# Kernel tuning notes

Measured on AMD Instinct MI355X. Metric: run time of the kernel, lower is better.

Reference implementation:

```python
import jax, jax.numpy as jnp
import numpy as np

B, H, W, C = 32, 56, 56, 192
NUM_HEADS = 6
WS = 7
SHIFT = 3
HIDDEN = 4 * C


def _relative_position_index(ws):
    coords = np.stack(np.meshgrid(np.arange(ws), np.arange(ws), indexing="ij"))  # 2,ws,ws
    coords = coords.reshape(2, -1)
    rel = coords[:, :, None] - coords[:, None, :]  # 2,N,N
    rel = rel.transpose(1, 2, 0)
    rel[:, :, 0] += ws - 1
    rel[:, :, 1] += ws - 1
    rel[:, :, 0] *= 2 * ws - 1
    return rel.sum(-1)  # N,N in [0, (2ws-1)^2)


def setup_inputs() -> dict:
    key = jax.random.key(0)
    ks = jax.random.split(key, 16)
    s = 0.02
    inp = {
        "x": jax.random.normal(ks[0], (B, H, W, C), jnp.float32),
        "norm1_g": jnp.ones((C,), jnp.float32),
        "norm1_b": jnp.zeros((C,), jnp.float32),
        "qkv_w": jax.random.normal(ks[1], (3 * C, C), jnp.float32) * s,
        "qkv_b": jnp.zeros((3 * C,), jnp.float32),
        "proj_w": jax.random.normal(ks[2], (C, C), jnp.float32) * s,
        "proj_b": jnp.zeros((C,), jnp.float32),
        "rel_bias_table": jax.random.normal(ks[3], ((2 * WS - 1) ** 2, NUM_HEADS), jnp.float32) * s,
        "norm2_g": jnp.ones((C,), jnp.float32),
        "norm2_b": jnp.zeros((C,), jnp.float32),
        "fc1_w": jax.random.normal(ks[4], (HIDDEN, C), jnp.float32) * s,
        "fc1_b": jnp.zeros((HIDDEN,), jnp.float32),
        "fc2_w": jax.random.normal(ks[5], (C, HIDDEN), jnp.float32) * s,
        "fc2_b": jnp.zeros((C,), jnp.float32),
        "rel_index": jnp.asarray(_relative_position_index(WS), jnp.int32),  # (49,49)
    }
    return inp


def _layernorm(x, g, b, eps=1e-5):
    mu = x.mean(-1, keepdims=True)
    var = ((x - mu) ** 2).mean(-1, keepdims=True)
    return (x - mu) * jax.lax.rsqrt(var + eps) * g + b


def _window_partition(x, ws):
    b, h, w, c = x.shape
    x = x.reshape(b, h // ws, ws, w // ws, ws, c)
    return x.transpose(0, 1, 3, 2, 4, 5).reshape(-1, ws * ws, c)


def _window_reverse(win, ws, b, h, w):
    c = win.shape[-1]
    x = win.reshape(b, h // ws, w // ws, ws, ws, c)
    return x.transpose(0, 1, 3, 2, 4, 5).reshape(b, h, w, c)


def reference(x, norm1_g, norm1_b, qkv_w, qkv_b, proj_w, proj_b, rel_bias_table,
              norm2_g, norm2_b, fc1_w, fc1_b, fc2_w, fc2_b, rel_index):
    shortcut = x
    xn = _layernorm(x, norm1_g, norm1_b)
    xs = jnp.roll(xn, (-SHIFT, -SHIFT), axis=(1, 2))
    win = _window_partition(xs, WS)  # (nW*B, 49, C)
    nw, n, c = win.shape
    hd = c // NUM_HEADS
    qkv = win @ qkv_w.T + qkv_b  # (nw, n, 3C)
    qkv = qkv.reshape(nw, n, 3, NUM_HEADS, hd).transpose(2, 0, 3, 1, 4)
    q, k, v = qkv[0], qkv[1], qkv[2]  # (nw, heads, n, hd)
    q = q * (hd ** -0.5)
    attn = jnp.einsum("whnd,whmd->whnm", q, k)
    bias = rel_bias_table[rel_index.reshape(-1)].reshape(n, n, NUM_HEADS).transpose(2, 0, 1)
    attn = jax.nn.softmax(attn + bias[None], axis=-1)
    out = jnp.einsum("whnm,whmd->whnd", attn, v)
    out = out.transpose(0, 2, 1, 3).reshape(nw, n, c)
    out = out @ proj_w.T + proj_b
    xs = _window_reverse(out, WS, x.shape[0], x.shape[1], x.shape[2])
    xa = jnp.roll(xs, (SHIFT, SHIFT), axis=(1, 2))
    x = shortcut + xa
    xm = _layernorm(x, norm2_g, norm2_b)
    xm = jax.nn.gelu(xm @ fc1_w.T + fc1_b, approximate=False)
    xm = xm @ fc2_w.T + fc2_b
    return x + xm
```

## Files before the change

kernel.cpp:

```cpp
#include <hip/hip_runtime.h>
#include <hip/hip_bf16.h>

#define CC 192
#define NHEADS 6
#define HDIM 32
#define NTOK 49
#define NWIN 2048
#define MTOK 100352
#define HIDDEN 768

typedef __hip_bfloat16 bf16;
typedef __attribute__((ext_vector_type(8))) short short8;
typedef __attribute__((ext_vector_type(4))) float f32x4;

__global__ __launch_bounds__(256) void k_wconv(
    const float* __restrict__ qw, const float* __restrict__ pw,
    const float* __restrict__ f1, const float* __restrict__ f2,
    bf16* __restrict__ o) {
  int i = blockIdx.x * 256 + threadIdx.x;
  if (i < 110592) o[i] = __float2bfloat16(qw[i]);
  else if (i < 147456) o[i] = __float2bfloat16(pw[i - 110592]);
  else if (i < 294912) o[i] = __float2bfloat16(f1[i - 147456]);
  else if (i < 442368) o[i] = __float2bfloat16(f2[i - 294912]);
}

__global__ __launch_bounds__(256) void k_bias(
    const float* __restrict__ table, const int* __restrict__ ridx,
    float* __restrict__ bias6) {
  int i = blockIdx.x * 256 + threadIdx.x;
  if (i >= 6 * 2401) return;
  int h = i / 2401, e = i - h * 2401;
  bias6[i] = table[ridx[e] * NHEADS + h];
}

template <int MODE, int NT, int KC, int MF>
__global__ __launch_bounds__(256) void k_gemm_areg(
    const void* __restrict__ Ap, const bf16* __restrict__ W,
    const float* __restrict__ bias, void* __restrict__ out0,
    const void* __restrict__ aux, const float* __restrict__ lng,
    const float* __restrict__ lnb) {
  constexpr int K = KC * 192;
  constexpr int N = NT * 64;
  __shared__ bf16 Bs[2][64 * 192];
  const int tid = threadIdx.x;
  const int wave = tid >> 6, lane = tid & 63;
  const int grp = lane >> 4, rA = lane & 15;
  const int cq = grp, cn = rA;
  const int m0 = blockIdx.x * (MF * 64);
  const int mrow = m0 + wave * (MF * 16);

  short8 areg[MF][KC * 6];
  if constexpr (MODE == 1) {
#pragma unroll
    for (int mt = 0; mt < MF; ++mt) {
      const bf16* arow =
          (const bf16*)Ap + (size_t)(mrow + mt * 16 + rA) * K + grp * 8;
#pragma unroll
      for (int kt = 0; kt < KC * 6; ++kt)
        areg[mt][kt] = *(const short8*)(arow + kt * 32);
    }
  } else {
#pragma unroll
    for (int mt = 0; mt < MF; ++mt) {
      int m = mrow + mt * 16 + rA;
      int w = m / 49, n = m - w * 49;
      int b = w >> 6, wrem = w & 63;
      int hi = wrem >> 3, wi = wrem & 7;
      int ii = n / 7, jj = n - ii * 7;
      int hs = hi * 7 + ii + 3; if (hs >= 56) hs -= 56;
      int wsc = wi * 7 + jj + 3; if (wsc >= 56) wsc -= 56;
      const float* rowp =
          (const float*)Ap + (size_t)((b * 56 + hs) * 56 + wsc) * CC;
      f32x4 xv[12];
#pragma unroll
      for (int kt = 0; kt < 6; ++kt) {
        xv[2 * kt]     = *(const f32x4*)(rowp + kt * 32 + grp * 8);
        xv[2 * kt + 1] = *(const f32x4*)(rowp + kt * 32 + grp * 8 + 4);
      }
      float s = 0.0f;
#pragma unroll
      for (int i = 0; i < 12; ++i)
#pragma unroll
        for (int j = 0; j < 4; ++j) s += xv[i][j];
      s += __shfl_xor(s, 16, 64);
      s += __shfl_xor(s, 32, 64);
      float mu = s * (1.0f / 192.0f);
      float q = 0.0f;
#pragma unroll
      for (int i = 0; i < 12; ++i)
#pragma unroll
        for (int j = 0; j < 4; ++j) {
          float d = xv[i][j] - mu;
          q += d * d;
        }
      q += __shfl_xor(q, 16, 64);
      q += __shfl_xor(q, 32, 64);
      float inv = rsqrtf(q * (1.0f / 192.0f) + 1e-5f);
#pragma unroll
      for (int kt = 0; kt < 6; ++kt) {
        short8 t;
#pragma unroll
        for (int j = 0; j < 8; ++j) {
          int col = kt * 32 + grp * 8 + j;
          float xval = xv[2 * kt + (j >> 2)][j & 3];
          float val = (xval - mu) * inv * lng[col] + lnb[col];
          bf16 hb = __float2bfloat16(val);
          t[j] = *reinterpret_cast<short*>(&hb);
        }
        areg[mt][kt] = t;
      }
    }
  }

  int rowoff[MF][4];
  if constexpr (MODE == 1) {
#pragma unroll
    for (int mt = 0; mt < MF; ++mt)
#pragma unroll
      for (int r = 0; r < 4; ++r) {
        int m = mrow + mt * 16 + cq * 4 + r;
        int w = m / 49, rr = m - w * 49;
        int b = w >> 6, wrem = w & 63;
        int hi = wrem >> 3, wi = wrem & 7;
        int ii = rr / 7, jj = rr - ii * 7;
        int hd = hi * 7 + ii + 3; if (hd >= 56) hd -= 56;
        int wd = wi * 7 + jj + 3; if (wd >= 56) wd -= 56;
        rowoff[mt][r] = ((b * 56 + hd) * 56 + wd) * CC;
      }
  }

  auto stage = [&](int buf, int nt, int kc) {
#pragma unroll
    for (int i = 0; i < 6; ++i) {
      int c = i * 256 + tid;
      int row = c / 24;
      int cbl = ((c - row * 24) * 16) ^ ((row & 7) << 4);
      const char* src = (const char*)W +
          (size_t)(nt * 64 + row) * (K * 2) + kc * 384 + cbl;
      __builtin_amdgcn_global_load_lds(
          (const __attribute__((address_space(1))) void*)src,
          (__attribute__((address_space(3))) void*)((char*)&Bs[buf][0] + c * 16),
          16, 0, 0);
    }
  };
  stage(0, 0, 0);

  f32x4 acc[MF][4];
#pragma unroll
  for (int s = 0; s < NT * KC; ++s) {
    const int nt = s / KC, kc = s - nt * KC;
    const int cur = s & 1;
    __syncthreads();
    if (s + 1 < NT * KC) stage(cur ^ 1, (s + 1) / KC, (s + 1) % KC);
    if (kc == 0) {
#pragma unroll
      for (int mt = 0; mt < MF; ++mt)
#pragma unroll
        for (int ntf = 0; ntf < 4; ++ntf)
          acc[mt][ntf] = (f32x4){0.f, 0.f, 0.f, 0.f};
    }
#pragma unroll
    for (int kt = 0; kt < 6; ++kt) {
      short8 b[4];
#pragma unroll
      for (int ntf = 0; ntf < 4; ++ntf) {
        int row = ntf * 16 + rA;
        int phys = row * 384 + ((kt * 64 + grp * 16) ^ ((row & 7) << 4));
        b[ntf] = *(const short8*)((const char*)&Bs[cur][0] + phys);
      }
#pragma unroll
      for (int mt = 0; mt < MF; ++mt)
#pragma unroll
        for (int ntf = 0; ntf < 4; ++ntf)
          acc[mt][ntf] = __builtin_amdgcn_mfma_f32_16x16x32_bf16(
              areg[mt][kc * 6 + kt], b[ntf], acc[mt][ntf], 0, 0, 0);
    }
    if (kc == KC - 1) {
      const int n0t = nt * 64;
      float bi[4];
#pragma unroll
      for (int ntf = 0; ntf < 4; ++ntf) bi[ntf] = bias[n0t + ntf * 16 + cn];
#pragma unroll
      for (int mt = 0; mt < MF; ++mt) {
#pragma unroll
        for (int r = 0; r < 4; ++r) {
          const int m = mrow + mt * 16 + cq * 4 + r;
#pragma unroll
          for (int ntf = 0; ntf < 4; ++ntf) {
            const int n = n0t + ntf * 16 + cn;
            float v = acc[mt][ntf][r] + bi[ntf];
            if constexpr (MODE == 0) {
              ((bf16*)out0)[(size_t)m * N + n] = __float2bfloat16(v);
            } else {
              float res = ((const float*)aux)[(size_t)rowoff[mt][r] + n];
              ((float*)out0)[(size_t)rowoff[mt][r] + n] = v + res;
            }
          }
        }
      }
    }
  }
}

__global__ __launch_bounds__(256) void k_mlp(
    const float* __restrict__ x1, const bf16* __restrict__ W1,
    const bf16* __restrict__ W2, const float* __restrict__ b1,
    const float* __restrict__ b2, float* __restrict__ out,
    const float* __restrict__ lng, const float* __restrict__ lnb) {
  __shared__ bf16 Bs[2][64 * 192];
  __shared__ bf16 Hl[4][16 * 72];
  const int tid = threadIdx.x;
  const int wave = tid >> 6, lane = tid & 63;
  const int grp = lane >> 4, rA = lane & 15;
  const int mrow = blockIdx.x * 64 + wave * 16;
  char* hb = (char*)&Hl[wave][0];

  short8 areg[6];
  {
    const float* rowp = x1 + (size_t)(mrow + rA) * CC;
    f32x4 xv[12];
#pragma unroll
    for (int kt = 0; kt < 6; ++kt) {
      xv[2 * kt]     = *(const f32x4*)(rowp + kt * 32 + grp * 8);
      xv[2 * kt + 1] = *(const f32x4*)(rowp + kt * 32 + grp * 8 + 4);
    }
    float s = 0.0f;
#pragma unroll
    for (int i = 0; i < 12; ++i)
#pragma unroll
      for (int j = 0; j < 4; ++j) s += xv[i][j];
    s += __shfl_xor(s, 16, 64);
    s += __shfl_xor(s, 32, 64);
    float mu = s * (1.0f / 192.0f);
    float q = 0.0f;
#pragma unroll
    for (int i = 0; i < 12; ++i)
#pragma unroll
      for (int j = 0; j < 4; ++j) {
        float d = xv[i][j] - mu;
        q += d * d;
      }
    q += __shfl_xor(q, 16, 64);
    q += __shfl_xor(q, 32, 64);
    float inv = rsqrtf(q * (1.0f / 192.0f) + 1e-5f);
#pragma unroll
    for (int kt = 0; kt < 6; ++kt) {
      short8 t;
#pragma unroll
      for (int j = 0; j < 8; ++j) {
        int col = kt * 32 + grp * 8 + j;
        float xval = xv[2 * kt + (j >> 2)][j & 3];
        float val = (xval - mu) * inv * lng[col] + lnb[col];
        bf16 hbv = __float2bfloat16(val);
        t[j] = *reinterpret_cast<short*>(&hbv);
      }
      areg[kt] = t;
    }
  }

  auto stage1 = [&](int c) {
#pragma unroll
    for (int i = 0; i < 6; ++i) {
      int cc = i * 256 + tid;
      int row = cc / 24;
      int cbl = ((cc - row * 24) * 16) ^ ((row & 7) << 4);
      const char* src = (const char*)W1 + (size_t)(c * 64 + row) * 384 + cbl;
      __builtin_amdgcn_global_load_lds(
          (const __attribute__((address_space(1))) void*)src,
          (__attribute__((address_space(3))) void*)((char*)&Bs[0][0] + cc * 16),
          16, 0, 0);
    }
  };
  auto stage2 = [&](int c) {
#pragma unroll
    for (int i = 0; i < 6; ++i) {
      int cc = i * 256 + tid;
      int row = cc >> 3, slot = cc & 7;
      int cbl = (slot * 16) ^ ((row & 7) << 4);
      const char* src = (const char*)W2 + (size_t)row * 1536 + c * 128 + cbl;
      __builtin_amdgcn_global_load_lds(
          (const __attribute__((address_space(1))) void*)src,
          (__attribute__((address_space(3))) void*)((char*)&Bs[1][0] + cc * 16),
          16, 0, 0);
    }
  };

  f32x4 acc2[12];
#pragma unroll
  for (int nf = 0; nf < 12; ++nf) acc2[nf] = (f32x4){0.f, 0.f, 0.f, 0.f};

  stage1(0);
  for (int c = 0; c < 12; ++c) {
    __syncthreads();
    stage2(c);
    f32x4 fa[4] = {};
#pragma unroll
    for (int kt = 0; kt < 6; ++kt) {
      short8 bfr[4];
#pragma unroll
      for (int ntf = 0; ntf < 4; ++ntf) {
        int row = ntf * 16 + rA;
        int phys = row * 384 + ((kt * 64 + grp * 16) ^ ((row & 7) << 4));
        bfr[ntf] = *(const short8*)((const char*)&Bs[0][0] + phys);
      }
#pragma unroll
      for (int ntf = 0; ntf < 4; ++ntf)
        fa[ntf] = __builtin_amdgcn_mfma_f32_16x16x32_bf16(
            areg[kt], bfr[ntf], fa[ntf], 0, 0, 0);
    }
#pragma unroll
    for (int ntf = 0; ntf < 4; ++ntf) {
      float b1v = b1[c * 64 + ntf * 16 + rA];
#pragma unroll
      for (int r = 0; r < 4; ++r) {
        float v = fa[ntf][r] + b1v;
        float u2 = 2.0f * v * (0.7978845608f + 0.0356774081f * v * v);
        float t = 1.0f - 2.0f / (1.0f + __expf(u2));
        float ge = 0.5f * v * (1.0f + t);
        int row = grp * 4 + r;
        int byte = (row * 144 + (ntf * 16 + rA) * 2) ^ ((row & 8) << 1);
        *(bf16*)(hb + byte) = __float2bfloat16(ge);
      }
    }
    __syncthreads();
    if (c + 1 < 12) stage1(c + 1);
    short8 a2[2];
#pragma unroll
    for (int kt2 = 0; kt2 < 2; ++kt2)
      a2[kt2] = *(const short8*)(
          hb + ((rA * 144 + grp * 16 + kt2 * 64) ^ ((rA & 8) << 1)));
#pragma unroll
    for (int nf = 0; nf < 12; ++nf) {
      int row = nf * 16 + rA;
      int sw = (row & 7) << 4;
      short8 bw0 = *(const short8*)(
          (const char*)&Bs[1][0] + row * 128 + ((grp * 16) ^ sw));
      short8 bw1 = *(const short8*)(
          (const char*)&Bs[1][0] + row * 128 + ((64 + grp * 16) ^ sw));
      acc2[nf] = __builtin_amdgcn_mfma_f32_16x16x32_bf16(a2[0], bw0, acc2[nf], 0, 0, 0);
      acc2[nf] = __builtin_amdgcn_mfma_f32_16x16x32_bf16(a2[1], bw1, acc2[nf], 0, 0, 0);
    }
  }

#pragma unroll
  for (int nf = 0; nf < 12; ++nf) {
    float b2v = b2[nf * 16 + rA];
#pragma unroll
    for (int r = 0; r < 4; ++r) {
      int m = mrow + grp * 4 + r;
      size_t idx = (size_t)m * CC + nf * 16 + rA;
      out[idx] = out[idx] + acc2[nf][r] + b2v;
    }
  }
}

__global__ __launch_bounds__(256) void k_attn_mfma(
    const bf16* __restrict__ qk, const float* __restrict__ bias6,
    bf16* __restrict__ ao) {
  __shared__ bf16 P[4][64 * 72];
  __shared__ bf16 VT[4][32 * 72];
  const int wave = threadIdx.x >> 6, lane = threadIdx.x & 63;
  const int wh = blockIdx.x * 4 + wave;
  const int w = wh / NHEADS, h = wh - w * NHEADS;
  const int rA = lane & 15, kq = (lane >> 4) * 8;
  const int grp = lane >> 4;

  const bf16* qbase = qk + (size_t)(w * 49) * 576 + h * HDIM + kq;

  short8 aq[4], bk[4], vrow[4];
#pragma unroll
  for (int t = 0; t < 4; ++t) {
    const bf16* rp = qbase + (size_t)(t * 16 + rA) * 576;
    aq[t] = *(const short8*)(rp);
    bk[t] = *(const short8*)(rp + 192);
    vrow[t] = *(const short8*)(rp + 384);
  }

  f32x4 S[4][4] = {};
#pragma unroll
  for (int mt = 0; mt < 4; ++mt)
#pragma unroll
    for (int nt = 0; nt < 4; ++nt)
      S[mt][nt] = __builtin_amdgcn_mfma_f32_16x16x32_bf16(
          aq[mt], bk[nt], S[mt][nt], 0, 0, 0);

  bf16* Vw = VT[wave];
  const bf16 zero = __float2bfloat16(0.0f);
#pragma unroll
  for (int t = 0; t < 4; ++t) {
    int tok = t * 16 + rA;
#pragma unroll
    for (int j = 0; j < 8; ++j)
      Vw[(kq + j) * 72 + tok] = (tok < 49) ? ((const bf16*)&vrow[t])[j] : zero;
  }

  const float scale = 0.17677669529663687f;
  const float* bh = bias6 + h * 2401;
  float rs[4][4];
  bf16* Pw = P[wave];
#pragma unroll
  for (int mt = 0; mt < 4; ++mt) {
#pragma unroll
    for (int r = 0; r < 4; ++r) {
      int row = mt * 16 + grp * 4 + r;
      float val[4];
#pragma unroll
      for (int nt = 0; nt < 4; ++nt) {
        int c = nt * 16 + rA;
        float bv = (row < 49 && c < 49) ? bh[row * 49 + c] : 0.0f;
        val[nt] = (c < 49) ? (S[mt][nt][r] * scale + bv) : -1e30f;
      }
      float mx = fmaxf(fmaxf(val[0], val[1]), fmaxf(val[2], val[3]));
      for (int m2 = 1; m2 < 16; m2 <<= 1) mx = fmaxf(mx, __shfl_xor(mx, m2, 64));
      float sum = 0.0f;
#pragma unroll
      for (int nt = 0; nt < 4; ++nt) {
        float e = __expf(val[nt] - mx);
        val[nt] = e;
        sum += e;
      }
      for (int m2 = 1; m2 < 16; m2 <<= 1) sum += __shfl_xor(sum, m2, 64);
      rs[mt][r] = 1.0f / sum;
#pragma unroll
      for (int nt = 0; nt < 4; ++nt)
        Pw[row * 72 + nt * 16 + rA] = __float2bfloat16(val[nt]);
    }
  }
  __syncthreads();

  short8 bv[2][2];
#pragma unroll
  for (int ks = 0; ks < 2; ++ks)
#pragma unroll
    for (int nt = 0; nt < 2; ++nt)
      bv[ks][nt] = *(const short8*)&Vw[(nt * 16 + rA) * 72 + ks * 32 + kq];
  f32x4 O[4][2] = {};
#pragma unroll
  for (int mt = 0; mt < 4; ++mt) {
    short8 ap0 = *(const short8*)&Pw[(mt * 16 + rA) * 72 + kq];
    short8 ap1 = *(const short8*)&Pw[(mt * 16 + rA) * 72 + 32 + kq];
#pragma unroll
    for (int nt = 0; nt < 2; ++nt) {
      O[mt][nt] = __builtin_amdgcn_mfma_f32_16x16x32_bf16(ap0, bv[0][nt],
                                                          O[mt][nt], 0, 0, 0);
      O[mt][nt] = __builtin_amdgcn_mfma_f32_16x16x32_bf16(ap1, bv[1][nt],
                                                          O[mt][nt], 0, 0, 0);
    }
  }
#pragma unroll
  for (int mt = 0; mt < 4; ++mt) {
#pragma unroll
    for (int r = 0; r < 4; ++r) {
      int m = mt * 16 + grp * 4 + r;
      if (m < 49) {
        bf16* orow = ao + (size_t)(w * 49 + m) * CC + h * HDIM;
#pragma unroll
        for (int nt = 0; nt < 2; ++nt)
          orow[nt * 16 + rA] = __float2bfloat16(O[mt][nt][r] * rs[mt][r]);
      }
    }
  }
}

extern "C" void kernel_launch(void* const* d_in, const int* in_sizes, int n_in,
                              void* d_out, int out_size, void* d_ws, size_t ws_size,
                              hipStream_t stream) {
  const float* x        = (const float*)d_in[0];
  const float* norm1_g  = (const float*)d_in[1];
  const float* norm1_b  = (const float*)d_in[2];
  const float* qkv_w    = (const float*)d_in[3];
  const float* qkv_b    = (const float*)d_in[4];
  const float* proj_w   = (const float*)d_in[5];
  const float* proj_b   = (const float*)d_in[6];
  const float* rel_tab  = (const float*)d_in[7];
  const float* norm2_g  = (const float*)d_in[8];
  const float* norm2_b  = (const float*)d_in[9];
  const float* fc1_w    = (const float*)d_in[10];
  const float* fc1_b    = (const float*)d_in[11];
  const float* fc2_w    = (const float*)d_in[12];
  const float* fc2_b    = (const float*)d_in[13];
  const int*   rel_idx  = (const int*)d_in[14];
  float* out = (float*)d_out;

  char* ws = (char*)d_ws;
  bf16*  qkb   = (bf16*)ws;
  bf16*  ao    = (bf16*)(ws + 115605504);
  bf16*  wbuf  = (bf16*)(ws + 154140672);
  float* bias6 = (float*)(ws + 155025408);
  float* x1    = out;
  bf16* wq = wbuf;
  bf16* wp = wbuf + 110592;
  bf16* w1 = wbuf + 147456;
  bf16* w2 = wbuf + 294912;

  k_wconv<<<1728, 256, 0, stream>>>(qkv_w, proj_w, fc1_w, fc2_w, wbuf);
  k_bias<<<57, 256, 0, stream>>>(rel_tab, rel_idx, bias6);
  k_gemm_areg<0, 9, 1, 1><<<MTOK / 64, 256, 0, stream>>>(
      x, wq, qkv_b, qkb, nullptr, norm1_g, norm1_b);
  k_attn_mfma<<<NWIN * NHEADS / 4, 256, 0, stream>>>(qkb, bias6, ao);
  k_gemm_areg<1, 3, 1, 2><<<MTOK / 128, 256, 0, stream>>>(
      ao, wp, proj_b, x1, x, nullptr, nullptr);
  k_mlp<<<MTOK / 64, 256, 0, stream>>>(
      x1, w1, w2, fc1_b, fc2_b, out, norm2_g, norm2_b);
}
```

Before: 451.9 us.

## Double M tile per wave in fused MLP, double-buffer W1, read W2 from global

After: 574.0 us. 27.0% more time.

```diff
diff --git a/kernel.cpp b/kernel.cpp
--- a/kernel.cpp
+++ b/kernel.cpp
@@ -202,22 +202,23 @@
   }
 }
 
-__global__ __launch_bounds__(256) void k_mlp(
+__global__ __launch_bounds__(256, 2) void k_mlp(
     const float* __restrict__ x1, const bf16* __restrict__ W1,
     const bf16* __restrict__ W2, const float* __restrict__ b1,
     const float* __restrict__ b2, float* __restrict__ out,
     const float* __restrict__ lng, const float* __restrict__ lnb) {
   __shared__ bf16 Bs[2][64 * 192];
-  __shared__ bf16 Hl[4][16 * 72];
+  __shared__ bf16 Hl[4][32 * 72];
   const int tid = threadIdx.x;
   const int wave = tid >> 6, lane = tid & 63;
   const int grp = lane >> 4, rA = lane & 15;
-  const int mrow = blockIdx.x * 64 + wave * 16;
+  const int mrow = blockIdx.x * 128 + wave * 32;
   char* hb = (char*)&Hl[wave][0];
 
-  short8 areg[6];
-  {
-    const float* rowp = x1 + (size_t)(mrow + rA) * CC;
+  short8 areg[2][6];
+#pragma unroll
+  for (int mt = 0; mt < 2; ++mt) {
+    const float* rowp = x1 + (size_t)(mrow + mt * 16 + rA) * CC;
     f32x4 xv[12];
 #pragma unroll
     for (int kt = 0; kt < 6; ++kt) {
@@ -254,11 +255,11 @@
         bf16 hbv = __float2bfloat16(val);
         t[j] = *reinterpret_cast<short*>(&hbv);
       }
-      areg[kt] = t;
-    }
-  }
-
-  auto stage1 = [&](int c) {
+      areg[mt][kt] = t;
+    }
+  }
+
+  auto stage1 = [&](int buf, int c) {
 #pragma unroll
     for (int i = 0; i < 6; ++i) {
       int cc = i * 256 + tid;
@@ -267,33 +268,23 @@
       const char* src = (const char*)W1 + (size_t)(c * 64 + row) * 384 + cbl;
       __builtin_amdgcn_global_load_lds(
           (const __attribute__((address_space(1))) void*)src,
-          (__attribute__((address_space(3))) void*)((char*)&Bs[0][0] + cc * 16),
+          (__attribute__((address_space(3))) void*)((char*)&Bs[buf][0] + cc * 16),
           16, 0, 0);
     }
   };
-  auto stage2 = [&](int c) {
-#pragma unroll
-    for (int i = 0; i < 6; ++i) {
-      int cc = i * 256 + tid;
-      int row = cc >> 3, slot = cc & 7;
-      int cbl = (slot * 16) ^ ((row & 7) << 4);
-      const char* src = (const char*)W2 + (size_t)row * 1536 + c * 128 + cbl;
-      __builtin_amdgcn_global_load_lds(
-          (const __attribute__((address_space(1))) void*)src,
-          (__attribute__((address_space(3))) void*)((char*)&Bs[1][0] + cc * 16),
-          16, 0, 0);
-    }
-  };
-
-  f32x4 acc2[12];
-#pragma unroll
-  for (int nf = 0; nf < 12; ++nf) acc2[nf] = (f32x4){0.f, 0.f, 0.f, 0.f};
-
-  stage1(0);
+
+  f32x4 acc2[2][12];
+#pragma unroll
+  for (int mt = 0; mt < 2; ++mt)
+#pragma unroll
+    for (int nf = 0; nf < 12; ++nf) acc2[mt][nf] = (f32x4){0.f, 0.f, 0.f, 0.f};
+
+  stage1(0, 0);
   for (int c = 0; c < 12; ++c) {
+    const int cur = c & 1;
     __syncthreads();
-    stage2(c);
-    f32x4 fa[4] = {};
+    if (c + 1 < 12) stage1(cur ^ 1, c + 1);
+    f32x4 fa[2][4] = {};
 #pragma unroll
     for (int kt = 0; kt < 6; ++kt) {
       short8 bfr[4];
@@ -301,44 +292,50 @@
       for (int ntf = 0; ntf < 4; ++ntf) {
         int row = ntf * 16 + rA;
         int phys = row * 384 + ((kt * 64 + grp * 16) ^ ((row & 7) << 4));
-        bfr[ntf] = *(const short8*)((const char*)&Bs[0][0] + phys);
-      }
-#pragma unroll
-      for (int ntf = 0; ntf < 4; ++ntf)
-        fa[ntf] = __builtin_amdgcn_mfma_f32_16x16x32_bf16(
-            areg[kt], bfr[ntf], fa[ntf], 0, 0, 0);
+        bfr[ntf] = *(const short8*)((const char*)&Bs[cur][0] + phys);
+      }
+#pragma unroll
+      for (int mt = 0; mt < 2; ++mt)
+#pragma unroll
+        for (int ntf = 0; ntf < 4; ++ntf)
+          fa[mt][ntf] = __builtin_amdgcn_mfma_f32_16x16x32_bf16(
+              areg[mt][kt], bfr[ntf], fa[mt][ntf], 0, 0, 0);
     }
 #pragma unroll
     for (int ntf = 0; ntf < 4; ++ntf) {
       float b1v = b1[c * 64 + ntf * 16 + rA];
 #pragma unroll
-      for (int r = 0; r < 4; ++r) {
-        float v = fa[ntf][r] + b1v;
-        float u2 = 2.0f * v * (0.7978845608f + 0.0356774081f * v * v);
-        float t = 1.0f - 2.0f / (1.0f + __expf(u2));
-        float ge = 0.5f * v * (1.0f + t);
-        int row = grp * 4 + r;
-        int byte = (row * 144 + (ntf * 16 + rA) * 2) ^ ((row & 8) << 1);
-        *(bf16*)(hb + byte) = __float2bfloat16(ge);
-      }
-    }
-    __syncthreads();
-    if (c + 1 < 12) stage1(c + 1);
-    short8 a2[2];
-#pragma unroll
-    for (int kt2 = 0; kt2 < 2; ++kt2)
-      a2[kt2] = *(const short8*)(
-          hb + ((rA * 144 + grp * 16 + kt2 * 64) ^ ((rA & 8) << 1)));
+      for (int mt = 0; mt < 2; ++mt) {
+#pragma unroll
+        for (int r = 0; r < 4; ++r) {
+          float v = fa[mt][ntf][r] + b1v;
+          float u2 = 2.0f * v * (0.7978845608f + 0.0356774081f * v * v);
+          float ge = v / (1.0f + __expf(-u2));
+          int row = mt * 16 + grp * 4 + r;
+          int byte = (row * 144 + (ntf * 16 + rA) * 2) ^ ((row & 8) << 1);
+          *(bf16*)(hb + byte) = __float2bfloat16(ge);
+        }
+      }
+    }
+    short8 a2[2][2];
+#pragma unroll
+    for (int mt = 0; mt < 2; ++mt)
+#pragma unroll
+      for (int kt2 = 0; kt2 < 2; ++kt2)
+        a2[mt][kt2] = *(const short8*)(
+            hb + (((mt * 16 + rA) * 144 + grp * 16 + kt2 * 64) ^ ((rA & 8) << 1)));
 #pragma unroll
     for (int nf = 0; nf < 12; ++nf) {
-      int row = nf * 16 + rA;
-      int sw = (row & 7) << 4;
-      short8 bw0 = *(const short8*)(
-          (const char*)&Bs[1][0] + row * 128 + ((grp * 16) ^ sw));
-      short8 bw1 = *(const short8*)(
-          (const char*)&Bs[1][0] + row * 128 + ((64 + grp * 16) ^ sw));
-      acc2[nf] = __builtin_amdgcn_mfma_f32_16x16x32_bf16(a2[0], bw0, acc2[nf], 0, 0, 0);
-      acc2[nf] = __builtin_amdgcn_mfma_f32_16x16x32_bf16(a2[1], bw1, acc2[nf], 0, 0, 0);
+      const bf16* wrow = W2 + (size_t)(nf * 16 + rA) * HIDDEN + c * 64 + grp * 8;
+      short8 bw0 = *(const short8*)(wrow);
+      short8 bw1 = *(const short8*)(wrow + 32);
+#pragma unroll
+      for (int mt = 0; mt < 2; ++mt) {
+        acc2[mt][nf] = __builtin_amdgcn_mfma_f32_16x16x32_bf16(
+            a2[mt][0], bw0, acc2[mt][nf], 0, 0, 0);
+        acc2[mt][nf] = __builtin_amdgcn_mfma_f32_16x16x32_bf16(
+            a2[mt][1], bw1, acc2[mt][nf], 0, 0, 0);
+      }
     }
   }
 
@@ -346,10 +343,13 @@
   for (int nf = 0; nf < 12; ++nf) {
     float b2v = b2[nf * 16 + rA];
 #pragma unroll
-    for (int r = 0; r < 4; ++r) {
-      int m = mrow + grp * 4 + r;
-      size_t idx = (size_t)m * CC + nf * 16 + rA;
-      out[idx] = out[idx] + acc2[nf][r] + b2v;
+    for (int mt = 0; mt < 2; ++mt) {
+#pragma unroll
+      for (int r = 0; r < 4; ++r) {
+        int m = mrow + mt * 16 + grp * 4 + r;
+        size_t idx = (size_t)m * CC + nf * 16 + rA;
+        out[idx] = out[idx] + acc2[mt][nf][r] + b2v;
+      }
     }
   }
 }
@@ -500,6 +500,6 @@
   k_attn_mfma<<<NWIN * NHEADS / 4, 256, 0, stream>>>(qkb, bias6, ao);
   k_gemm_areg<1, 3, 1, 2><<<MTOK / 128, 256, 0, stream>>>(
       ao, wp, proj_b, x1, x, nullptr, nullptr);
-  k_mlp<<<MTOK / 64, 256, 0, stream>>>(
+  k_mlp<<<MTOK / 128, 256, 0, stream>>>(
       x1, w1, w2, fc1_b, fc2_b, out, norm2_g, norm2_b);
 }
```

## Double-buffer fused MLP weight chunks with smaller hidden slices and one barrier

Applied to the files above, without the earlier changes.

Result: slower. 463.4 us (+2.6%).

```diff
diff --git a/kernel.cpp b/kernel.cpp
--- a/kernel.cpp
+++ b/kernel.cpp
@@ -207,8 +207,9 @@
     const bf16* __restrict__ W2, const float* __restrict__ b1,
     const float* __restrict__ b2, float* __restrict__ out,
     const float* __restrict__ lng, const float* __restrict__ lnb) {
-  __shared__ bf16 Bs[2][64 * 192];
-  __shared__ bf16 Hl[4][16 * 72];
+  __shared__ bf16 W1s[2][32 * 192];
+  __shared__ bf16 W2s[2][192 * 32];
+  __shared__ bf16 Hl[4][640];
   const int tid = threadIdx.x;
   const int wave = tid >> 6, lane = tid & 63;
   const int grp = lane >> 4, rA = lane & 15;
@@ -258,29 +259,29 @@
     }
   }
 
-  auto stage1 = [&](int c) {
-#pragma unroll
-    for (int i = 0; i < 6; ++i) {
-      int cc = i * 256 + tid;
-      int row = cc / 24;
-      int cbl = ((cc - row * 24) * 16) ^ ((row & 7) << 4);
-      const char* src = (const char*)W1 + (size_t)(c * 64 + row) * 384 + cbl;
+  auto stage1 = [&](int buf, int c) {
+#pragma unroll
+    for (int i = 0; i < 3; ++i) {
+      int s = i * 256 + tid;
+      int row = s / 24, slot = s - row * 24;
+      int cbl = (slot * 16) ^ ((row & 7) << 4);
+      const char* src = (const char*)W1 + (size_t)(c * 32 + row) * 384 + cbl;
       __builtin_amdgcn_global_load_lds(
           (const __attribute__((address_space(1))) void*)src,
-          (__attribute__((address_space(3))) void*)((char*)&Bs[0][0] + cc * 16),
+          (__attribute__((address_space(3))) void*)((char*)&W1s[buf][0] + s * 16),
           16, 0, 0);
     }
   };
-  auto stage2 = [&](int c) {
-#pragma unroll
-    for (int i = 0; i < 6; ++i) {
-      int cc = i * 256 + tid;
-      int row = cc >> 3, slot = cc & 7;
-      int cbl = (slot * 16) ^ ((row & 7) << 4);
-      const char* src = (const char*)W2 + (size_t)row * 1536 + c * 128 + cbl;
+  auto stage2 = [&](int buf, int c) {
+#pragma unroll
+    for (int i = 0; i < 3; ++i) {
+      int s = i * 256 + tid;
+      int row = s >> 2, slot = s & 3;
+      int cbl = (slot * 16) ^ (((row >> 1) & 3) << 4);
+      const char* src = (const char*)W2 + (size_t)row * 1536 + c * 64 + cbl;
       __builtin_amdgcn_global_load_lds(
           (const __attribute__((address_space(1))) void*)src,
-          (__attribute__((address_space(3))) void*)((char*)&Bs[1][0] + cc * 16),
+          (__attribute__((address_space(3))) void*)((char*)&W2s[buf][0] + s * 16),
           16, 0, 0);
     }
   };
@@ -289,56 +290,47 @@
 #pragma unroll
   for (int nf = 0; nf < 12; ++nf) acc2[nf] = (f32x4){0.f, 0.f, 0.f, 0.f};
 
-  stage1(0);
-  for (int c = 0; c < 12; ++c) {
+  stage1(0, 0);
+  stage2(0, 0);
+  for (int c = 0; c < 24; ++c) {
+    const int cur = c & 1;
     __syncthreads();
-    stage2(c);
-    f32x4 fa[4] = {};
+    if (c + 1 < 24) { stage1(cur ^ 1, c + 1); stage2(cur ^ 1, c + 1); }
+    f32x4 fa[2] = {};
 #pragma unroll
     for (int kt = 0; kt < 6; ++kt) {
-      short8 bfr[4];
-#pragma unroll
-      for (int ntf = 0; ntf < 4; ++ntf) {
+      short8 bfr[2];
+#pragma unroll
+      for (int ntf = 0; ntf < 2; ++ntf) {
         int row = ntf * 16 + rA;
         int phys = row * 384 + ((kt * 64 + grp * 16) ^ ((row & 7) << 4));
-        bfr[ntf] = *(const short8*)((const char*)&Bs[0][0] + phys);
-      }
-#pragma unroll
-      for (int ntf = 0; ntf < 4; ++ntf)
+        bfr[ntf] = *(const short8*)((const char*)&W1s[cur][0] + phys);
+      }
+#pragma unroll
+      for (int ntf = 0; ntf < 2; ++ntf)
         fa[ntf] = __builtin_amdgcn_mfma_f32_16x16x32_bf16(
             areg[kt], bfr[ntf], fa[ntf], 0, 0, 0);
     }
 #pragma unroll
-    for (int ntf = 0; ntf < 4; ++ntf) {
-      float b1v = b1[c * 64 + ntf * 16 + rA];
+    for (int ntf = 0; ntf < 2; ++ntf) {
+      float b1v = b1[c * 32 + ntf * 16 + rA];
 #pragma unroll
       for (int r = 0; r < 4; ++r) {
         float v = fa[ntf][r] + b1v;
         float u2 = 2.0f * v * (0.7978845608f + 0.0356774081f * v * v);
-        float t = 1.0f - 2.0f / (1.0f + __expf(u2));
-        float ge = 0.5f * v * (1.0f + t);
+        float ge = v / (1.0f + __expf(-u2));
         int row = grp * 4 + r;
-        int byte = (row * 144 + (ntf * 16 + rA) * 2) ^ ((row & 8) << 1);
-        *(bf16*)(hb + byte) = __float2bfloat16(ge);
-      }
-    }
-    __syncthreads();
-    if (c + 1 < 12) stage1(c + 1);
-    short8 a2[2];
-#pragma unroll
-    for (int kt2 = 0; kt2 < 2; ++kt2)
-      a2[kt2] = *(const short8*)(
-          hb + ((rA * 144 + grp * 16 + kt2 * 64) ^ ((rA & 8) << 1)));
+        *(bf16*)(hb + row * 80 + (ntf * 16 + rA) * 2) = __float2bfloat16(ge);
+      }
+    }
+    short8 a2 = *(const short8*)(hb + rA * 80 + grp * 16);
 #pragma unroll
     for (int nf = 0; nf < 12; ++nf) {
       int row = nf * 16 + rA;
-      int sw = (row & 7) << 4;
-      short8 bw0 = *(const short8*)(
-          (const char*)&Bs[1][0] + row * 128 + ((grp * 16) ^ sw));
-      short8 bw1 = *(const short8*)(
-          (const char*)&Bs[1][0] + row * 128 + ((64 + grp * 16) ^ sw));
-      acc2[nf] = __builtin_amdgcn_mfma_f32_16x16x32_bf16(a2[0], bw0, acc2[nf], 0, 0, 0);
-      acc2[nf] = __builtin_amdgcn_mfma_f32_16x16x32_bf16(a2[1], bw1, acc2[nf], 0, 0, 0);
+      int phys = row * 64 + ((grp * 16) ^ (((row >> 1) & 3) << 4));
+      short8 bw = *(const short8*)((const char*)&W2s[cur][0] + phys);
+      acc2[nf] = __builtin_amdgcn_mfma_f32_16x16x32_bf16(a2, bw, acc2[nf],
+                                                         0, 0, 0);
     }
   }
 
```
